# Kernel tuning notes

Hardware: AMD Instinct MI355X
Metric: run time of the kernel (lower is better)

## Reference

```python
import jax, jax.numpy as jnp
import numpy as np

B = 4096
D = 512
TEMPERATURE = 0.07


def setup_inputs() -> dict:
    key = jax.random.key(0)
    k1, k2 = jax.random.split(key)
    logits = jax.random.normal(k1, (B, D), dtype=jnp.float32)
    label = jax.random.normal(k2, (B, D), dtype=jnp.float32)
    return {"logits": logits, "label": label}


def reference(logits, label):
    # concat the two views -> [2B, D]
    feats = jnp.concatenate([logits, label], axis=0)
    n = feats.shape[0]
    b = n // 2
    # L2 normalize along feature dim (F.normalize, eps for safety)
    norm = jnp.maximum(jnp.linalg.norm(feats, axis=1, keepdims=True), 1e-12)
    feats = feats / norm
    # similarity matrix [2B, 2B]
    sim = jnp.matmul(feats, feats.T) / TEMPERATURE
    idx = jnp.arange(n)
    # positive pair of row i is row (i + B) mod 2B
    pos = sim[idx, (idx + b) % n]
    # CrossEntropy with target 0 over [pos, negatives] == masked LSE - pos.
    # Mask out the diagonal (self-similarity), which the torch code removes
    # via the boolean-eye mask before building logits.
    neg_inf = jnp.array(-jnp.inf, dtype=sim.dtype)
    sim_masked = jnp.where(idx[:, None] == idx[None, :], neg_inf, sim)
    lse = jax.nn.logsumexp(sim_masked, axis=1)
    loss = jnp.mean(lse - pos)
    return loss
```

## Files before the change

### kernel.cpp

```cpp
#include <hip/hip_runtime.h>
#include <hip/hip_bf16.h>

#define NROWS 8192
#define BHALF 4096
#define DDIM  512

#define BM 128
#define BK 64
#define NT (NROWS / BM)
#define NTRI (NT * (NT + 1) / 2)

#define FSCALE 3.7796447300922722f

typedef short bf16x8 __attribute__((ext_vector_type(8)));
typedef float f32x4 __attribute__((ext_vector_type(4)));
typedef unsigned short u16x8 __attribute__((ext_vector_type(8)));
typedef __attribute__((address_space(1))) unsigned int gu32;
typedef __attribute__((address_space(3))) unsigned int lu32;

__global__ __launch_bounds__(256) void normalize_kernel(
    const float* __restrict__ logits, const float* __restrict__ label,
    unsigned short* __restrict__ fn) {
  const int w = threadIdx.x >> 6, lane = threadIdx.x & 63;
  const int row = blockIdx.x * 4 + w;
  const float* src = (row < BHALF) ? (logits + (size_t)row * DDIM)
                                   : (label + (size_t)(row - BHALF) * DDIM);
  const float4* s4 = (const float4*)src;
  float4 a = s4[lane * 2 + 0];
  float4 b = s4[lane * 2 + 1];
  float ss = a.x * a.x + a.y * a.y + a.z * a.z + a.w * a.w +
             b.x * b.x + b.y * b.y + b.z * b.z + b.w * b.w;
#pragma unroll
  for (int m = 1; m < 64; m <<= 1) ss += __shfl_xor(ss, m);
  const float inv = FSCALE / fmaxf(sqrtf(ss), 1e-12f);
  const float v[8] = {a.x, a.y, a.z, a.w, b.x, b.y, b.z, b.w};
  u16x8 o;
#pragma unroll
  for (int j = 0; j < 8; ++j) {
    float x = v[j] * inv;
    unsigned u = __float_as_uint(x);
    unsigned r = (u + 0x7fffu + ((u >> 16) & 1u)) >> 16;
    o[j] = (unsigned short)r;
  }
  *(u16x8*)(fn + (size_t)row * DDIM + lane * 8) = o;
}

__global__ __launch_bounds__(256) void simexp_tri_kernel(
    const unsigned short* __restrict__ fn, float* __restrict__ rowsum,
    float* __restrict__ pos) {
  __shared__ unsigned short ldsA[BM * BK];
  __shared__ unsigned short ldsB[BM * BK];
  __shared__ float lds_rsum[BM];
  __shared__ float lds_csum[BM];

  const int u = (NTRI - 1) - (int)blockIdx.x;
  int k = (int)((sqrtf(8.f * (float)u + 1.f) - 1.f) * 0.5f);
  while ((k + 1) * (k + 2) / 2 <= u) ++k;
  while (k * (k + 1) / 2 > u) --k;
  const int rm = (NT - 1) - k;
  const int cn = (NT - 1) - (u - k * (k + 1) / 2);
  const int rowBase = rm * BM, colBase = cn * BM;
  const bool diag = (rm == cn);
  const bool posTile = (cn == rm + NT / 2);

  const int tid = threadIdx.x;
  const int w = tid >> 6, lane = tid & 63;
  const int wr = w >> 1, wc = w & 1;
  const int l15 = lane & 15, l4 = lane >> 4;

  if (tid < BM) { lds_rsum[tid] = 0.f; lds_csum[tid] = 0.f; }

  const int r8 = lane >> 3;
  const int sgbyte = ((lane & 7) ^ r8) * 16;

  f32x4 acc[4][4];
#pragma unroll
  for (int m = 0; m < 4; ++m)
#pragma unroll
    for (int n = 0; n < 4; ++n) acc[m][n] = (f32x4){0.f, 0.f, 0.f, 0.f};

  for (int kk = 0; kk < DDIM; kk += BK) {
    __syncthreads();
#pragma unroll
    for (int i = 0; i < 4; ++i) {
      const int seg = w * 4 + i;
      const int row = seg * 8 + r8;
      const char* gA = (const char*)(fn + (size_t)(rowBase + row) * DDIM + kk) + sgbyte;
      const char* gB = (const char*)(fn + (size_t)(colBase + row) * DDIM + kk) + sgbyte;
      __builtin_amdgcn_global_load_lds((gu32*)gA, (lu32*)((char*)ldsA + seg * 1024), 16, 0, 0);
      __builtin_amdgcn_global_load_lds((gu32*)gB, (lu32*)((char*)ldsB + seg * 1024), 16, 0, 0);
    }
    __syncthreads();
#pragma unroll
    for (int ks = 0; ks < 2; ++ks) {
      bf16x8 af[4], bfr[4];
#pragma unroll
      for (int m = 0; m < 4; ++m) {
        const int r = wr * 64 + m * 16 + l15;
        af[m] = *(const bf16x8*)((const char*)ldsA + r * 128 + (((ks * 4 + l4) ^ (r & 7)) << 4));
      }
#pragma unroll
      for (int n = 0; n < 4; ++n) {
        const int r = wc * 64 + n * 16 + l15;
        bfr[n] = *(const bf16x8*)((const char*)ldsB + r * 128 + (((ks * 4 + l4) ^ (r & 7)) << 4));
      }
#pragma unroll
      for (int m = 0; m < 4; ++m)
#pragma unroll
        for (int n = 0; n < 4; ++n)
          acc[m][n] = __builtin_amdgcn_mfma_f32_16x16x32_bf16(af[m], bfr[n], acc[m][n], 0, 0, 0);
    }
  }

  float rs[4][4];
  float cs[4];
#pragma unroll
  for (int m = 0; m < 4; ++m)
#pragma unroll
    for (int j = 0; j < 4; ++j) rs[m][j] = 0.f;
#pragma unroll
  for (int n = 0; n < 4; ++n) cs[n] = 0.f;

#pragma unroll
  for (int m = 0; m < 4; ++m)
#pragma unroll
    for (int n = 0; n < 4; ++n)
#pragma unroll
      for (int j = 0; j < 4; ++j) {
        const int rl = wr * 64 + m * 16 + l4 * 4 + j;
        const int cl = wc * 64 + n * 16 + l15;
        const float v = acc[m][n][j];
        float e = __expf(v);
        if (diag && rl == cl) e = 0.f;
        rs[m][j] += e;
        cs[n] += e;
        if (posTile && rl == cl) pos[rowBase + rl] = v;
      }

#pragma unroll
  for (int m = 0; m < 4; ++m)
#pragma unroll
    for (int j = 0; j < 4; ++j) {
      float s = rs[m][j];
      s += __shfl_xor(s, 1);
      s += __shfl_xor(s, 2);
      s += __shfl_xor(s, 4);
      s += __shfl_xor(s, 8);
      if (l15 == 0) atomicAdd(&lds_rsum[wr * 64 + m * 16 + l4 * 4 + j], s);
    }
  if (!diag) {
#pragma unroll
    for (int n = 0; n < 4; ++n) {
      float s = cs[n];
      s += __shfl_xor(s, 16);
      s += __shfl_xor(s, 32);
      if (l4 == 0) atomicAdd(&lds_csum[wc * 64 + n * 16 + l15], s);
    }
  }
  __syncthreads();
  if (tid < BM) {
    atomicAdd(&rowsum[rowBase + tid], lds_rsum[tid]);
    if (!diag) atomicAdd(&rowsum[colBase + tid], lds_csum[tid]);
  }
}

__global__ __launch_bounds__(1024) void reduce_kernel(
    const float* __restrict__ rowsum, const float* __restrict__ pos,
    float* __restrict__ out) {
  __shared__ float part[16];
  float a = 0.f;
  for (int i = threadIdx.x; i < NROWS; i += 1024)
    a += __logf(rowsum[i]) - pos[i & (BHALF - 1)];
#pragma unroll
  for (int m = 1; m < 64; m <<= 1) a += __shfl_xor(a, m);
  const int w = threadIdx.x >> 6, lane = threadIdx.x & 63;
  if (lane == 0) part[w] = a;
  __syncthreads();
  if (threadIdx.x == 0) {
    float t = 0.f;
#pragma unroll
    for (int i = 0; i < 16; ++i) t += part[i];
    out[0] = t * (1.0f / NROWS);
  }
}

extern "C" void kernel_launch(void* const* d_in, const int* in_sizes, int n_in,
                              void* d_out, int out_size, void* d_ws, size_t ws_size,
                              hipStream_t stream) {
  const float* logits = (const float*)d_in[0];
  const float* label = (const float*)d_in[1];
  float* out = (float*)d_out;
  unsigned short* fn = (unsigned short*)d_ws;
  float* rowsum = (float*)((char*)d_ws + (size_t)NROWS * DDIM * 2);
  float* pos = rowsum + NROWS;

  hipMemsetAsync(rowsum, 0, NROWS * sizeof(float), stream);
  normalize_kernel<<<NROWS / 4, 256, 0, stream>>>(logits, label, fn);
  simexp_tri_kernel<<<NTRI, 256, 0, stream>>>(fn, rowsum, pos);
  reduce_kernel<<<1, 1024, 0, stream>>>(rowsum, pos, out);
}
```

Baseline: 139.6 us.

## Double-buffer LDS tiles, remap blocks across XCDs, fold memset, parallelize reduce

The GEMM-exp kernel now double-buffers its A/B LDS tiles, so the global-to-LDS loads for the next K step are issued before computing the current one, hiding load latency. Block IDs are remapped so that consecutive triangle tiles land on the same XCD group, which should improve L2 locality. The rowsum memset is folded into the normalize kernel, removing one launch. The final reduction now spans 32 blocks that combine through an atomic add. The cost is doubled LDS per block (64KB), which may lower occupancy, and a float atomic ordering that is no longer deterministic.

```diff
diff --git a/kernel.cpp b/kernel.cpp
--- a/kernel.cpp
+++ b/kernel.cpp
@@ -7,8 +7,10 @@
 
 #define BM 128
 #define BK 64
+#define KSTEPS (DDIM / BK)
 #define NT (NROWS / BM)
 #define NTRI (NT * (NT + 1) / 2)
+#define CPX (NTRI / 8)
 
 #define FSCALE 3.7796447300922722f
 
@@ -20,7 +22,13 @@
 
 __global__ __launch_bounds__(256) void normalize_kernel(
     const float* __restrict__ logits, const float* __restrict__ label,
-    unsigned short* __restrict__ fn) {
+    unsigned short* __restrict__ fn, float* __restrict__ rowsum,
+    float* __restrict__ out) {
+  if (blockIdx.x < 8)
+    ((float4*)rowsum)[blockIdx.x * 256 + threadIdx.x] =
+        make_float4(0.f, 0.f, 0.f, 0.f);
+  if (blockIdx.x == 8 && threadIdx.x == 0) out[0] = 0.f;
+
   const int w = threadIdx.x >> 6, lane = threadIdx.x & 63;
   const int row = blockIdx.x * 4 + w;
   const float* src = (row < BHALF) ? (logits + (size_t)row * DDIM)
@@ -48,12 +56,14 @@
 __global__ __launch_bounds__(256) void simexp_tri_kernel(
     const unsigned short* __restrict__ fn, float* __restrict__ rowsum,
     float* __restrict__ pos) {
-  __shared__ unsigned short ldsA[BM * BK];
-  __shared__ unsigned short ldsB[BM * BK];
+  __shared__ unsigned short ldsA[2][BM * BK];
+  __shared__ unsigned short ldsB[2][BM * BK];
   __shared__ float lds_rsum[BM];
   __shared__ float lds_csum[BM];
 
-  const int u = (NTRI - 1) - (int)blockIdx.x;
+  const int bid0 = (int)blockIdx.x;
+  const int bid = (bid0 & 7) * CPX + (bid0 >> 3);
+  const int u = (NTRI - 1) - bid;
   int k = (int)((sqrtf(8.f * (float)u + 1.f) - 1.f) * 0.5f);
   while ((k + 1) * (k + 2) / 2 <= u) ++k;
   while (k * (k + 1) / 2 > u) --k;
@@ -73,43 +83,63 @@
   const int r8 = lane >> 3;
   const int sgbyte = ((lane & 7) ^ r8) * 16;
 
-  f32x4 acc[4][4];
-#pragma unroll
-  for (int m = 0; m < 4; ++m)
-#pragma unroll
-    for (int n = 0; n < 4; ++n) acc[m][n] = (f32x4){0.f, 0.f, 0.f, 0.f};
-
-  for (int kk = 0; kk < DDIM; kk += BK) {
-    __syncthreads();
+  auto stage = [&](unsigned short* dA, unsigned short* dB, int kk) {
 #pragma unroll
     for (int i = 0; i < 4; ++i) {
       const int seg = w * 4 + i;
       const int row = seg * 8 + r8;
-      const char* gA = (const char*)(fn + (size_t)(rowBase + row) * DDIM + kk) + sgbyte;
-      const char* gB = (const char*)(fn + (size_t)(colBase + row) * DDIM + kk) + sgbyte;
-      __builtin_amdgcn_global_load_lds((gu32*)gA, (lu32*)((char*)ldsA + seg * 1024), 16, 0, 0);
-      __builtin_amdgcn_global_load_lds((gu32*)gB, (lu32*)((char*)ldsB + seg * 1024), 16, 0, 0);
-    }
-    __syncthreads();
+      const char* gA =
+          (const char*)(fn + (size_t)(rowBase + row) * DDIM + kk) + sgbyte;
+      const char* gB =
+          (const char*)(fn + (size_t)(colBase + row) * DDIM + kk) + sgbyte;
+      __builtin_amdgcn_global_load_lds((gu32*)gA,
+                                       (lu32*)((char*)dA + seg * 1024), 16, 0, 0);
+      __builtin_amdgcn_global_load_lds((gu32*)gB,
+                                       (lu32*)((char*)dB + seg * 1024), 16, 0, 0);
+    }
+  };
+
+  f32x4 acc[4][4];
+#pragma unroll
+  for (int m = 0; m < 4; ++m)
+#pragma unroll
+    for (int n = 0; n < 4; ++n) acc[m][n] = (f32x4){0.f, 0.f, 0.f, 0.f};
+
+  auto compute = [&](const unsigned short* sA, const unsigned short* sB) {
 #pragma unroll
     for (int ks = 0; ks < 2; ++ks) {
       bf16x8 af[4], bfr[4];
 #pragma unroll
       for (int m = 0; m < 4; ++m) {
         const int r = wr * 64 + m * 16 + l15;
-        af[m] = *(const bf16x8*)((const char*)ldsA + r * 128 + (((ks * 4 + l4) ^ (r & 7)) << 4));
+        af[m] = *(const bf16x8*)((const char*)sA + r * 128 +
+                                 (((ks * 4 + l4) ^ (r & 7)) << 4));
       }
 #pragma unroll
       for (int n = 0; n < 4; ++n) {
         const int r = wc * 64 + n * 16 + l15;
-        bfr[n] = *(const bf16x8*)((const char*)ldsB + r * 128 + (((ks * 4 + l4) ^ (r & 7)) << 4));
+        bfr[n] = *(const bf16x8*)((const char*)sB + r * 128 +
+                                  (((ks * 4 + l4) ^ (r & 7)) << 4));
       }
 #pragma unroll
       for (int m = 0; m < 4; ++m)
 #pragma unroll
         for (int n = 0; n < 4; ++n)
-          acc[m][n] = __builtin_amdgcn_mfma_f32_16x16x32_bf16(af[m], bfr[n], acc[m][n], 0, 0, 0);
-    }
+          acc[m][n] = __builtin_amdgcn_mfma_f32_16x16x32_bf16(af[m], bfr[n],
+                                                              acc[m][n], 0, 0, 0);
+    }
+  };
+
+  stage(ldsA[0], ldsB[0], 0);
+  __syncthreads();
+#pragma unroll
+  for (int t = 0; t < KSTEPS; t += 2) {
+    if (t + 1 < KSTEPS) stage(ldsA[1], ldsB[1], (t + 1) * BK);
+    compute(ldsA[0], ldsB[0]);
+    __syncthreads();
+    if (t + 2 < KSTEPS) stage(ldsA[0], ldsB[0], (t + 2) * BK);
+    compute(ldsA[1], ldsB[1]);
+    __syncthreads();
   }
 
   float rs[4][4];
@@ -164,24 +194,19 @@
   }
 }
 
-__global__ __launch_bounds__(1024) void reduce_kernel(
+__global__ __launch_bounds__(256) void reduce_kernel(
     const float* __restrict__ rowsum, const float* __restrict__ pos,
     float* __restrict__ out) {
-  __shared__ float part[16];
-  float a = 0.f;
-  for (int i = threadIdx.x; i < NROWS; i += 1024)
-    a += __logf(rowsum[i]) - pos[i & (BHALF - 1)];
+  __shared__ float part[4];
+  const int i = blockIdx.x * 256 + threadIdx.x;
+  float a = __logf(rowsum[i]) - pos[i & (BHALF - 1)];
 #pragma unroll
   for (int m = 1; m < 64; m <<= 1) a += __shfl_xor(a, m);
   const int w = threadIdx.x >> 6, lane = threadIdx.x & 63;
   if (lane == 0) part[w] = a;
   __syncthreads();
-  if (threadIdx.x == 0) {
-    float t = 0.f;
-#pragma unroll
-    for (int i = 0; i < 16; ++i) t += part[i];
-    out[0] = t * (1.0f / NROWS);
-  }
+  if (threadIdx.x == 0)
+    atomicAdd(out, (part[0] + part[1] + part[2] + part[3]) * (1.0f / NROWS));
 }
 
 extern "C" void kernel_launch(void* const* d_in, const int* in_sizes, int n_in,
@@ -194,8 +219,7 @@
   float* rowsum = (float*)((char*)d_ws + (size_t)NROWS * DDIM * 2);
   float* pos = rowsum + NROWS;
 
-  hipMemsetAsync(rowsum, 0, NROWS * sizeof(float), stream);
-  normalize_kernel<<<NROWS / 4, 256, 0, stream>>>(logits, label, fn);
+  normalize_kernel<<<NROWS / 4, 256, 0, stream>>>(logits, label, fn, rowsum, out);
   simexp_tri_kernel<<<NTRI, 256, 0, stream>>>(fn, rowsum, pos);
-  reduce_kernel<<<1, 1024, 0, stream>>>(rowsum, pos, out);
-}
+  reduce_kernel<<<NROWS / 256, 256, 0, stream>>>(rowsum, pos, out);
+}
```

New measurement: 137.2 us. Within noise of the previous version (-1.7%).
